# Kernel tuning notes

Measured on AMD Instinct MI355X. Metric: run time of the kernel, lower is better.

Reference implementation:

```python
import jax, jax.numpy as jnp
import numpy as np

TAU = 0.07
EPS = 1e-6  # torch CosineSimilarity eps


def setup_inputs() -> dict:
    key = jax.random.key(0)
    k1, k2, k3 = jax.random.split(key, 3)
    n, d, n_classes = 8192, 256, 1024
    imitation_embeds = jax.random.normal(k1, (n, d), dtype=jnp.float32)
    recording_embeds = jax.random.normal(k2, (n, d), dtype=jnp.float32)
    labels = jax.random.randint(k3, (n,), 0, n_classes, dtype=jnp.int64)
    return {
        "imitation_embeds": imitation_embeds,
        "recording_embeds": recording_embeds,
        "labels": labels,
    }


def reference(imitation_embeds, recording_embeds, labels):
    n = imitation_embeds.shape[0]
    # cosine similarity with per-vector norm clamp (torch semantics)
    im_n = imitation_embeds / jnp.maximum(
        jnp.linalg.norm(imitation_embeds, axis=1, keepdims=True), EPS)
    rec_n = recording_embeds / jnp.maximum(
        jnp.linalg.norm(recording_embeds, axis=1, keepdims=True), EPS)
    i2r = jnp.einsum("nd,md->nm", im_n, rec_n) / TAU  # [n, n]

    same = labels[:, None] == labels[None, :]          # [n, n] bool
    eye = jnp.eye(n, dtype=bool)
    # original: mask = ~(same ^ diag_embed(diag(same))); diag(same) is all True
    # -> keep the diagonal (positive) and all different-label negatives
    mask = ~(same ^ eye)

    # per-row masked log-softmax evaluated at the diagonal entry:
    # log_softmax(row[mask])[pos_of_diag] = i2r[i,i] - logsumexp(row over mask)
    lse = jax.nn.logsumexp(jnp.where(mask, i2r, -jnp.inf), axis=1)  # [n]
    loss = -jnp.mean(jnp.diagonal(i2r) - lse)
    return loss
```

## Files before the change

### kernel.cpp

```cpp
#include <hip/hip_runtime.h>

#define N 8192
#define D 256
#define INV_TAU 14.285714285714286f
#define LOG2E 1.4426950408889634f
#define EPSN 1e-6f

#define RT 256
#define CT 64
#define CSPLIT 16
#define CPB (N / CSPLIT)
#define NTILES (CPB / CT)
#define MAXC 96

typedef unsigned int u32x4 __attribute__((ext_vector_type(4)));
typedef __bf16 bf16x8 __attribute__((ext_vector_type(8)));
typedef float f32x4 __attribute__((ext_vector_type(4)));

__device__ inline unsigned short f2bf(float x) {
    unsigned int u = __builtin_bit_cast(unsigned int, x);
    u += 0x7fffu + ((u >> 16) & 1u);
    return (unsigned short)(u >> 16);
}

__device__ inline float bf2f(unsigned short u) {
    return __builtin_bit_cast(float, (unsigned int)u << 16);
}

__global__ void ntx_prep(const float* __restrict__ im, const float* __restrict__ rec,
                         const int* __restrict__ labels,
                         unsigned short* __restrict__ A, unsigned short* __restrict__ Bm,
                         float* __restrict__ diag, float* __restrict__ rowsum,
                         int* __restrict__ cnt, int* __restrict__ bucket,
                         float* __restrict__ out) {
    const int wave = threadIdx.x >> 6;
    const int lane = threadIdx.x & 63;
    const int row  = blockIdx.x * 4 + wave;

    const float4 a = ((const float4*)(im  + (size_t)row * D))[lane];
    const float4 b = ((const float4*)(rec + (size_t)row * D))[lane];

    float ssa = a.x*a.x + a.y*a.y + a.z*a.z + a.w*a.w;
    float ssb = b.x*b.x + b.y*b.y + b.z*b.z + b.w*b.w;
    float dt  = a.x*b.x + a.y*b.y + a.z*b.z + a.w*b.w;
    #pragma unroll
    for (int o = 32; o; o >>= 1) {
        ssa += __shfl_xor(ssa, o);
        ssb += __shfl_xor(ssb, o);
        dt  += __shfl_xor(dt , o);
    }
    const float ra = 1.0f / fmaxf(sqrtf(ssa), EPSN);
    const float rb = 1.0f / fmaxf(sqrtf(ssb), EPSN);
    const float sa = ra * (INV_TAU * LOG2E);

    ushort4 pa, pb;
    pa.x = f2bf(a.x*sa); pa.y = f2bf(a.y*sa); pa.z = f2bf(a.z*sa); pa.w = f2bf(a.w*sa);
    pb.x = f2bf(b.x*rb); pb.y = f2bf(b.y*rb); pb.z = f2bf(b.z*rb); pb.w = f2bf(b.w*rb);
    *(ushort4*)(A  + (size_t)row * D + lane * 4) = pa;
    *(ushort4*)(Bm + (size_t)row * D + lane * 4) = pb;

    if (lane == 0) {
        diag[row]   = dt * ra * rb * INV_TAU;
        rowsum[row] = 0.0f;
        const int c = labels[row];
        const int pos = atomicAdd(&cnt[c], 1);
        if (pos < MAXC) bucket[c * MAXC + pos] = row;
    }
    if (blockIdx.x == 0 && threadIdx.x == 0) out[0] = 0.0f;
}

__device__ __forceinline__ void stage_tile(const unsigned short* gs, unsigned char* lb) {
    #pragma unroll
    for (int p = 0; p < 8; ++p)
        __builtin_amdgcn_global_load_lds(
            (const __attribute__((address_space(1))) unsigned int*)(gs + p * 32),
            (__attribute__((address_space(3))) unsigned int*)(lb + p * 1024),
            16, 0, 0);
}

__global__ __launch_bounds__(256, 2)
void ntx_lse(const unsigned short* __restrict__ A, const unsigned short* __restrict__ Bm,
             float* __restrict__ rowsum) {
    __shared__ __align__(128) unsigned char Bs[2][CT * 512];

    const int wave = threadIdx.x >> 6;
    const int lane = threadIdx.x & 63;
    const int g    = lane >> 4;
    const int n16  = lane & 15;

    const int rowblk = blockIdx.x & (N / RT - 1);
    const int colblk = blockIdx.x >> 5;
    const int row0 = rowblk * RT + wave * 64;
    const int col0 = colblk * CPB;

    bf16x8 afrag[4][8];
    #pragma unroll
    for (int rs = 0; rs < 4; ++rs) {
        const int r = row0 + rs * 16 + n16;
        #pragma unroll
        for (int k = 0; k < 8; ++k)
            afrag[rs][k] = __builtin_bit_cast(
                bf16x8, *(const u32x4*)(A + (size_t)r * D + k * 32 + g * 8));
    }

    float acc[4][4];
    #pragma unroll
    for (int rs = 0; rs < 4; ++rs)
        #pragma unroll
        for (int q = 0; q < 4; ++q) acc[rs][q] = 0.f;

    const unsigned short* gsrc0 = Bm + (size_t)(col0 + wave * 16 + n16) * D + g * 8;
    unsigned char* lds0 = &Bs[0][wave * 8192];
    unsigned char* lds1 = &Bs[1][wave * 8192];

    stage_tile(gsrc0, lds0);
    asm volatile("s_waitcnt vmcnt(0)" ::: "memory");
    __builtin_amdgcn_s_barrier();
    __builtin_amdgcn_sched_barrier(0);

    for (int t = 0; t < NTILES; ++t) {
        const int buf = t & 1;
        if (t + 1 < NTILES)
            stage_tile(gsrc0 + (size_t)(t + 1) * CT * D, buf ? lds0 : lds1);

        #pragma unroll
        for (int cs = 0; cs < 4; ++cs) {
            bf16x8 bfrag[8];
            #pragma unroll
            for (int k = 0; k < 8; ++k)
                bfrag[k] = __builtin_bit_cast(
                    bf16x8, *(const u32x4*)(&Bs[buf][(cs * 8 + k) * 1024 + lane * 16]));

            #pragma unroll
            for (int rs = 0; rs < 4; ++rs) {
                f32x4 c = {0.f, 0.f, 0.f, 0.f};
                #pragma unroll
                for (int k = 0; k < 8; ++k)
                    c = __builtin_amdgcn_mfma_f32_16x16x32_bf16(
                            afrag[rs][k], bfrag[k], c, 0, 0, 0);
                #pragma unroll
                for (int q = 0; q < 4; ++q)
                    acc[rs][q] += __builtin_amdgcn_exp2f(c[q]);
            }
        }

        asm volatile("s_waitcnt vmcnt(0)" ::: "memory");
        __builtin_amdgcn_s_barrier();
        __builtin_amdgcn_sched_barrier(0);
    }

    #pragma unroll
    for (int rs = 0; rs < 4; ++rs)
        #pragma unroll
        for (int q = 0; q < 4; ++q) {
            float v = acc[rs][q];
            v += __shfl_xor(v, 1);
            v += __shfl_xor(v, 2);
            v += __shfl_xor(v, 4);
            v += __shfl_xor(v, 8);
            if (n16 == 0)
                atomicAdd(&rowsum[row0 + rs * 16 + g * 4 + q], v);
        }
}

__global__ void ntx_pfin(const unsigned short* __restrict__ A,
                         const unsigned short* __restrict__ Bm,
                         const int* __restrict__ labels,
                         const int* __restrict__ cnt, const int* __restrict__ bucket,
                         const float* __restrict__ diag, const float* __restrict__ rowsum,
                         float* __restrict__ out) {
    __shared__ float red[4];
    const int wave = threadIdx.x >> 6;
    const int lane = threadIdx.x & 63;
    const int i = blockIdx.x * 4 + wave;
    const int c = labels[i];
    const int m = min(cnt[c], MAXC);

    float corr = 0.f;
    if (m >= 2) {
        const ushort4 av = *(const ushort4*)(A + (size_t)i * D + lane * 4);
        const float a0 = bf2f(av.x), a1 = bf2f(av.y), a2 = bf2f(av.z), a3 = bf2f(av.w);

        int jr_n = bucket[c * MAXC];
        ushort4 bv_n = *(const ushort4*)(Bm + (size_t)jr_n * D + lane * 4);

        for (int j = 0; j < m; ++j) {
            const int jr = jr_n;
            const ushort4 bv = bv_n;
            if (j + 1 < m) {
                jr_n = bucket[c * MAXC + j + 1];
                bv_n = *(const ushort4*)(Bm + (size_t)jr_n * D + lane * 4);
            }
            if (jr == i) continue;
            float d = a0*bf2f(bv.x) + a1*bf2f(bv.y) + a2*bf2f(bv.z) + a3*bf2f(bv.w);
            #pragma unroll
            for (int o = 32; o; o >>= 1) d += __shfl_xor(d, o);
            corr += __builtin_amdgcn_exp2f(d);
        }
    }
    if (lane == 0) red[wave] = logf(rowsum[i] - corr) - diag[i];
    __syncthreads();
    if (threadIdx.x == 0)
        atomicAdd(out, (red[0] + red[1] + red[2] + red[3]) * (1.0f / (float)N));
}

extern "C" void kernel_launch(void* const* d_in, const int* in_sizes, int n_in,
                              void* d_out, int out_size, void* d_ws, size_t ws_size,
                              hipStream_t stream) {
    const float* im     = (const float*)d_in[0];
    const float* rec    = (const float*)d_in[1];
    const int*   labels = (const int*)d_in[2];
    float* out = (float*)d_out;

    unsigned short* A  = (unsigned short*)d_ws;
    unsigned short* Bm = A + (size_t)N * D;
    float* diag   = (float*)(Bm + (size_t)N * D);
    float* rowsum = diag + N;
    int*   cnt    = (int*)(rowsum + N);
    int*   bucket = cnt + 1024;

    hipMemsetAsync(cnt, 0, 1024 * sizeof(int), stream);
    ntx_prep<<<N / 4, 256, 0, stream>>>(im, rec, labels, A, Bm, diag, rowsum, cnt, bucket, out);
    ntx_lse<<<(N / RT) * CSPLIT, 256, 0, stream>>>(A, Bm, rowsum);
    ntx_pfin<<<N / 4, 256, 0, stream>>>(A, Bm, labels, cnt, bucket, diag, rowsum, out);
}
```

Before: 141.0 us.

## Split label bucketing and pair correction into separate kernels, drop memset

Replaces the hipMemsetAsync with zeroing of the class counters inside the prep kernel. Label bucketing moves to its own small kernel, and the same-label correction becomes a pairs kernel that subtracts its sum from rowsum atomically before the main GEMM/exp kernel runs. Finalisation becomes a tiny per-row log-and-reduce kernel. This removes a memset call and makes the final kernel trivial, at the cost of two extra kernel launches and an extra atomic per row on rowsum.

```diff
diff --git a/kernel.cpp b/kernel.cpp
--- a/kernel.cpp
+++ b/kernel.cpp
@@ -28,11 +28,9 @@
 }
 
 __global__ void ntx_prep(const float* __restrict__ im, const float* __restrict__ rec,
-                         const int* __restrict__ labels,
                          unsigned short* __restrict__ A, unsigned short* __restrict__ Bm,
                          float* __restrict__ diag, float* __restrict__ rowsum,
-                         int* __restrict__ cnt, int* __restrict__ bucket,
-                         float* __restrict__ out) {
+                         int* __restrict__ cnt, float* __restrict__ out) {
     const int wave = threadIdx.x >> 6;
     const int lane = threadIdx.x & 63;
     const int row  = blockIdx.x * 4 + wave;
@@ -62,11 +60,52 @@
     if (lane == 0) {
         diag[row]   = dt * ra * rb * INV_TAU;
         rowsum[row] = 0.0f;
-        const int c = labels[row];
-        const int pos = atomicAdd(&cnt[c], 1);
-        if (pos < MAXC) bucket[c * MAXC + pos] = row;
-    }
+    }
+    if (blockIdx.x < 4) cnt[blockIdx.x * 256 + threadIdx.x] = 0;
     if (blockIdx.x == 0 && threadIdx.x == 0) out[0] = 0.0f;
+}
+
+__global__ void ntx_bucket(const int* __restrict__ labels, int* __restrict__ cnt,
+                           int* __restrict__ bucket) {
+    const int i = blockIdx.x * 256 + threadIdx.x;
+    const int c = labels[i];
+    const int pos = atomicAdd(&cnt[c], 1);
+    if (pos < MAXC) bucket[c * MAXC + pos] = i;
+}
+
+__global__ void ntx_pairs(const unsigned short* __restrict__ A,
+                          const unsigned short* __restrict__ Bm,
+                          const int* __restrict__ labels,
+                          const int* __restrict__ cnt, const int* __restrict__ bucket,
+                          float* __restrict__ rowsum) {
+    const int wave = threadIdx.x >> 6;
+    const int lane = threadIdx.x & 63;
+    const int i = blockIdx.x * 4 + wave;
+    const int c = labels[i];
+    const int m = min(cnt[c], MAXC);
+    if (m < 2) return;
+
+    const ushort4 av = *(const ushort4*)(A + (size_t)i * D + lane * 4);
+    const float a0 = bf2f(av.x), a1 = bf2f(av.y), a2 = bf2f(av.z), a3 = bf2f(av.w);
+
+    int jr_n = bucket[c * MAXC];
+    ushort4 bv_n = *(const ushort4*)(Bm + (size_t)jr_n * D + lane * 4);
+
+    float corr = 0.f;
+    for (int j = 0; j < m; ++j) {
+        const int jr = jr_n;
+        const ushort4 bv = bv_n;
+        if (j + 1 < m) {
+            jr_n = bucket[c * MAXC + j + 1];
+            bv_n = *(const ushort4*)(Bm + (size_t)jr_n * D + lane * 4);
+        }
+        if (jr == i) continue;
+        float d = a0*bf2f(bv.x) + a1*bf2f(bv.y) + a2*bf2f(bv.z) + a3*bf2f(bv.w);
+        #pragma unroll
+        for (int o = 32; o; o >>= 1) d += __shfl_xor(d, o);
+        corr += __builtin_amdgcn_exp2f(d);
+    }
+    if (lane == 0) atomicAdd(&rowsum[i], -corr);
 }
 
 __device__ __forceinline__ void stage_tile(const unsigned short* gs, unsigned char* lb) {
@@ -163,42 +202,15 @@
         }
 }
 
-__global__ void ntx_pfin(const unsigned short* __restrict__ A,
-                         const unsigned short* __restrict__ Bm,
-                         const int* __restrict__ labels,
-                         const int* __restrict__ cnt, const int* __restrict__ bucket,
-                         const float* __restrict__ diag, const float* __restrict__ rowsum,
-                         float* __restrict__ out) {
+__global__ void ntx_finish(const float* __restrict__ diag,
+                           const float* __restrict__ rowsum,
+                           float* __restrict__ out) {
     __shared__ float red[4];
-    const int wave = threadIdx.x >> 6;
-    const int lane = threadIdx.x & 63;
-    const int i = blockIdx.x * 4 + wave;
-    const int c = labels[i];
-    const int m = min(cnt[c], MAXC);
-
-    float corr = 0.f;
-    if (m >= 2) {
-        const ushort4 av = *(const ushort4*)(A + (size_t)i * D + lane * 4);
-        const float a0 = bf2f(av.x), a1 = bf2f(av.y), a2 = bf2f(av.z), a3 = bf2f(av.w);
-
-        int jr_n = bucket[c * MAXC];
-        ushort4 bv_n = *(const ushort4*)(Bm + (size_t)jr_n * D + lane * 4);
-
-        for (int j = 0; j < m; ++j) {
-            const int jr = jr_n;
-            const ushort4 bv = bv_n;
-            if (j + 1 < m) {
-                jr_n = bucket[c * MAXC + j + 1];
-                bv_n = *(const ushort4*)(Bm + (size_t)jr_n * D + lane * 4);
-            }
-            if (jr == i) continue;
-            float d = a0*bf2f(bv.x) + a1*bf2f(bv.y) + a2*bf2f(bv.z) + a3*bf2f(bv.w);
-            #pragma unroll
-            for (int o = 32; o; o >>= 1) d += __shfl_xor(d, o);
-            corr += __builtin_amdgcn_exp2f(d);
-        }
-    }
-    if (lane == 0) red[wave] = logf(rowsum[i] - corr) - diag[i];
+    const int i = blockIdx.x * 256 + threadIdx.x;
+    float s = logf(rowsum[i]) - diag[i];
+    #pragma unroll
+    for (int o = 32; o; o >>= 1) s += __shfl_xor(s, o);
+    if ((threadIdx.x & 63) == 0) red[threadIdx.x >> 6] = s;
     __syncthreads();
     if (threadIdx.x == 0)
         atomicAdd(out, (red[0] + red[1] + red[2] + red[3]) * (1.0f / (float)N));
@@ -219,8 +231,9 @@
     int*   cnt    = (int*)(rowsum + N);
     int*   bucket = cnt + 1024;
 
-    hipMemsetAsync(cnt, 0, 1024 * sizeof(int), stream);
-    ntx_prep<<<N / 4, 256, 0, stream>>>(im, rec, labels, A, Bm, diag, rowsum, cnt, bucket, out);
+    ntx_prep<<<N / 4, 256, 0, stream>>>(im, rec, A, Bm, diag, rowsum, cnt, out);
+    ntx_bucket<<<N / 256, 256, 0, stream>>>(labels, cnt, bucket);
+    ntx_pairs<<<N / 4, 256, 0, stream>>>(A, Bm, labels, cnt, bucket, rowsum);
     ntx_lse<<<(N / RT) * CSPLIT, 256, 0, stream>>>(A, Bm, rowsum);
-    ntx_pfin<<<N / 4, 256, 0, stream>>>(A, Bm, labels, cnt, bucket, diag, rowsum, out);
-}
+    ntx_finish<<<N / 256, 256, 0, stream>>>(diag, rowsum, out);
+}
```

New measurement: 121.8 us. 13.6% less time.
